# Kernel tuning notes

Measured on AMD Instinct MI355X. Metric: run time of the kernel, lower is better.

Reference implementation:

```python
import jax, jax.numpy as jnp
import numpy as np

B, Q, K, F, H, D = 2, 4096, 4096, 512, 8, 64

def setup_inputs() -> dict:
    key = jax.random.key(0)
    ks = jax.random.split(key, 6)
    s = 1.0 / np.sqrt(F)
    return {
        "inputs_q": jax.random.normal(ks[0], (B, Q, F), dtype=jnp.float32),
        "inputs_kv": jax.random.normal(ks[1], (B, K, F), dtype=jnp.float32),
        "Wq": jax.random.normal(ks[2], (F, H, D), dtype=jnp.float32) * s,
        "Wk": jax.random.normal(ks[3], (F, H, D), dtype=jnp.float32) * s,
        "Wv": jax.random.normal(ks[4], (F, H, D), dtype=jnp.float32) * s,
        "Wo": jax.random.normal(ks[5], (H, D, F), dtype=jnp.float32) * (1.0 / np.sqrt(H * D)),
    }

def reference(inputs_q, inputs_kv, Wq, Wk, Wv, Wo):
    # QKV projections (DenseGeneral, no bias): [B, L, F] -> [B, L, H, D]
    q = jnp.einsum("bqf,fhd->bqhd", inputs_q, Wq)
    k = jnp.einsum("bkf,fhd->bkhd", inputs_kv, Wk)
    v = jnp.einsum("bkf,fhd->bkhd", inputs_kv, Wv)
    # Explicit attention matrix [B, H, Q, K] as in the original module
    logits = jnp.einsum("bqhd,bkhd->bhqk", q, k)
    attn = jax.nn.softmax(logits, axis=-1)
    out = jnp.einsum("bhqk,bkhd->bqhd", attn, v)
    # Output projection over (heads, head_dim): [B, Q, H, D] -> [B, Q, F]
    return jnp.einsum("bqhd,hdf->bqf", out, Wo)
```

## Files before the change

### kernel.cpp

```cpp
#include <hip/hip_runtime.h>
#include <hip/hip_bf16.h>

typedef short bf16x8 __attribute__((ext_vector_type(8)));
typedef _Float16 f16;
typedef f16 f16x8 __attribute__((ext_vector_type(8)));
typedef float f32x4 __attribute__((ext_vector_type(4)));
typedef unsigned short u16;
typedef u16 u16x8 __attribute__((ext_vector_type(8)));
typedef unsigned int u32;
typedef u32 u32x2 __attribute__((ext_vector_type(2)));

#define B_  2
#define L_  4096
#define F_  512
#define H_  8
#define D_  64
#define M_  8192
#define NSPL 2
#define KHALF (L_ / NSPL)

#define LOG2E 1.442695041f

__device__ inline u16 f2bf(float f) {
    union { float f; unsigned u; } v; v.f = f;
    unsigned r = v.u + 0x7fff + ((v.u >> 16) & 1);
    return (u16)(r >> 16);
}
__device__ inline u16 f2h(float f) {
    union { f16 h; u16 u; } v; v.h = (f16)f;
    return v.u;
}
__device__ inline float h2f(u16 u) {
    union { u16 u; f16 h; } v; v.u = u;
    return (float)v.h;
}

__global__ __launch_bounds__(256) void wt_kernel(
    const float* __restrict__ Wq, const float* __restrict__ Wk,
    const float* __restrict__ Wv, const float* __restrict__ Wo,
    u16* __restrict__ Tq, u16* __restrict__ Tk,
    u16* __restrict__ Tv, u16* __restrict__ To) {
    __shared__ float t[32][33];
    const int z = blockIdx.z;
    const float* in = (z == 0) ? Wq : (z == 1) ? Wk : (z == 2) ? Wv : Wo;
    u16* out = (z == 0) ? Tq : (z == 1) ? Tk : (z == 2) ? Tv : To;
    int k0 = blockIdx.y * 32, n0 = blockIdx.x * 32;
    int c = threadIdx.x & 31, r8 = threadIdx.x >> 5;
#pragma unroll
    for (int i = 0; i < 4; ++i) {
        int r = r8 * 4 + i;
        t[r][c] = in[(size_t)(k0 + r) * F_ + n0 + c];
    }
    __syncthreads();
#pragma unroll
    for (int i = 0; i < 4; ++i) {
        int r = r8 * 4 + i;
        out[(size_t)(n0 + r) * F_ + k0 + c] = f2h(t[c][r]);
    }
}

__global__ __launch_bounds__(256, 3) void proj_kernel(
    const float* __restrict__ Xq, const float* __restrict__ Xkv,
    const u16* __restrict__ Wqt, const u16* __restrict__ Wkt,
    const u16* __restrict__ Wvt,
    u16* __restrict__ Qw, u16* __restrict__ Kw, u16* __restrict__ Vw) {
    __shared__ u16 Ah[128][72];
    __shared__ u16 B1[64][72];
    const int tid = threadIdx.x;
    const int w = tid >> 6, lane = tid & 63, lx = lane & 15, quad = lane >> 4;
    const int m0 = blockIdx.x * 128, n0 = blockIdx.y * 64;
    const int z = blockIdx.z;
    const float* A = (z == 0) ? Xq : Xkv;
    const u16* W1 = (z == 0) ? Wqt : (z == 1) ? Wkt : Wvt;

    float4 apre[8];
    u16x8 b1p[2];

    auto load_ab = [&](int k0) {
#pragma unroll
        for (int it = 0; it < 4; ++it) {
            int slot = tid + it * 256, r = slot >> 3, g = (slot & 7) * 8;
            apre[2 * it]     = *(const float4*)(A + (size_t)(m0 + r) * F_ + k0 + g);
            apre[2 * it + 1] = *(const float4*)(A + (size_t)(m0 + r) * F_ + k0 + g + 4);
        }
#pragma unroll
        for (int it = 0; it < 2; ++it) {
            int slot = tid + it * 256, r = slot >> 3, g = (slot & 7) * 8;
            b1p[it] = *(const u16x8*)(W1 + (size_t)(n0 + r) * F_ + k0 + g);
        }
    };
    auto write_ab = [&]() {
#pragma unroll
        for (int it = 0; it < 4; ++it) {
            int slot = tid + it * 256, r = slot >> 3, g = (slot & 7) * 8;
            float4 f0 = apre[2 * it], f1 = apre[2 * it + 1];
            u16 th[8] = {f2h(f0.x), f2h(f0.y), f2h(f0.z), f2h(f0.w),
                         f2h(f1.x), f2h(f1.y), f2h(f1.z), f2h(f1.w)};
            *(u16x8*)&Ah[r][g] = *(u16x8*)th;
        }
#pragma unroll
        for (int it = 0; it < 2; ++it) {
            int slot = tid + it * 256, r = slot >> 3, g = (slot & 7) * 8;
            *(u16x8*)&B1[r][g] = b1p[it];
        }
    };

    f32x4 acc1[2][4] = {};

    load_ab(0);
    write_ab();
    __syncthreads();
    load_ab(64);

    for (int k0 = 0; k0 < F_; k0 += 64) {
#pragma unroll
        for (int ks = 0; ks < 2; ++ks) {
            f16x8 af[2];
#pragma unroll
            for (int mf = 0; mf < 2; ++mf)
                af[mf] = *(const f16x8*)&Ah[w * 32 + mf * 16 + lx][ks * 32 + quad * 8];
#pragma unroll
            for (int nt = 0; nt < 4; ++nt) {
                f16x8 b1 = *(const f16x8*)&B1[nt * 16 + lx][ks * 32 + quad * 8];
#pragma unroll
                for (int mf = 0; mf < 2; ++mf)
                    acc1[mf][nt] = __builtin_amdgcn_mfma_f32_16x16x32_f16(af[mf], b1, acc1[mf][nt], 0, 0, 0);
            }
        }
        if (k0 < F_ - 64) {
            __syncthreads();
            write_ab();
            __syncthreads();
            if (k0 < F_ - 128) load_ab(k0 + 128);
        }
    }

    const int h = n0 >> 6;
    if (z < 2) {
        const float scl = (z == 0) ? LOG2E : 1.0f;
        u16* C1 = (z == 0) ? Qw : Kw;
#pragma unroll
        for (int mf = 0; mf < 2; ++mf)
#pragma unroll
            for (int nt = 0; nt < 4; ++nt)
#pragma unroll
                for (int i = 0; i < 4; ++i) {
                    int m = m0 + w * 32 + mf * 16 + quad * 4 + i;
                    int b = m >> 12, l = m & 4095;
                    int d = nt * 16 + lx;
                    C1[((size_t)(b * H_ + h) * L_ + l) * D_ + d] = f2h(acc1[mf][nt][i] * scl);
                }
    } else {
        __syncthreads();
#pragma unroll
        for (int mf = 0; mf < 2; ++mf)
#pragma unroll
            for (int nt = 0; nt < 4; ++nt)
#pragma unroll
                for (int i = 0; i < 4; ++i)
                    Ah[w * 32 + mf * 16 + quad * 4 + i][nt * 16 + lx] = f2bf(acc1[mf][nt][i]);
        __syncthreads();
        int d = tid >> 2, seg = (tid & 3) * 32;
        int b = m0 >> 12;
        u16 tmp[32];
#pragma unroll
        for (int j = 0; j < 32; ++j) tmp[j] = Ah[seg + j][d];
        size_t base = ((size_t)(b * H_ + h) * D_ + d) * L_ + (m0 & 4095) + seg;
#pragma unroll
        for (int c = 0; c < 4; ++c)
            *(u16x8*)(Vw + base + c * 8) = *(u16x8*)&tmp[c * 8];
    }
}

__global__ __launch_bounds__(256) void out_gemm(const u16* __restrict__ A16,
                                                const u16* __restrict__ Wt,
                                                float* __restrict__ Cf) {
    __shared__ u16 As[128][72];
    __shared__ u16 Bs[128][72];
    const int tid = threadIdx.x;
    const int w = tid >> 6, lane = tid & 63, lx = lane & 15, quad = lane >> 4;
    const int m0 = blockIdx.x * 128, n0 = blockIdx.y * 128;

    u16x8 a16p[4];
    u16x8 bp[4];

    auto load_ab = [&](int k0) {
#pragma unroll
        for (int it = 0; it < 4; ++it) {
            int slot = tid + it * 256, r = slot >> 3, g = (slot & 7) * 8;
            a16p[it] = *(const u16x8*)(A16 + (size_t)(m0 + r) * F_ + k0 + g);
            bp[it]   = *(const u16x8*)(Wt  + (size_t)(n0 + r) * F_ + k0 + g);
        }
    };
    auto write_ab = [&]() {
#pragma unroll
        for (int it = 0; it < 4; ++it) {
            int slot = tid + it * 256, r = slot >> 3, g = (slot & 7) * 8;
            *(u16x8*)&As[r][g] = a16p[it];
            *(u16x8*)&Bs[r][g] = bp[it];
        }
    };

    f32x4 acc[2][8] = {};

    load_ab(0);
    write_ab();
    __syncthreads();
    load_ab(64);

    for (int k0 = 0; k0 < F_; k0 += 64) {
#pragma unroll
        for (int ks = 0; ks < 2; ++ks) {
            f16x8 af[2];
#pragma unroll
            for (int mf = 0; mf < 2; ++mf)
                af[mf] = *(const f16x8*)&As[w * 32 + mf * 16 + lx][ks * 32 + quad * 8];
#pragma unroll
            for (int nt = 0; nt < 8; ++nt) {
                f16x8 bf = *(const f16x8*)&Bs[nt * 16 + lx][ks * 32 + quad * 8];
#pragma unroll
                for (int mf = 0; mf < 2; ++mf)
                    acc[mf][nt] = __builtin_amdgcn_mfma_f32_16x16x32_f16(af[mf], bf, acc[mf][nt], 0, 0, 0);
            }
        }
        if (k0 < F_ - 64) {
            __syncthreads();
            write_ab();
            __syncthreads();
            if (k0 < F_ - 128) load_ab(k0 + 128);
        }
    }

#pragma unroll
    for (int mf = 0; mf < 2; ++mf)
#pragma unroll
        for (int nt = 0; nt < 8; ++nt)
#pragma unroll
            for (int i = 0; i < 4; ++i) {
                int m = m0 + w * 32 + mf * 16 + quad * 4 + i;
                int n = n0 + nt * 16 + lx;
                Cf[(size_t)m * F_ + n] = acc[mf][nt][i];
            }
}

__global__ __launch_bounds__(256, 2) void flash_mfma(
    const u16* __restrict__ Qg, const u16* __restrict__ Kg,
    const u16* __restrict__ Vtg, u16* __restrict__ On, float* __restrict__ Ls) {
    __shared__ u16 Ks[2][64][72];
    __shared__ u16 Vs[2][64][72];

    const int tid = threadIdx.x;
    const int w = tid >> 6, lane = tid & 63, lx = lane & 15, quad = lane >> 4;

    const int x = blockIdx.x;
    const int t = x >> 3;
    const int hh = t >> 5;
    const int s = (t >> 4) & 1;
    const int bh = (x & 7) * 2 + hh;
    const int q0 = (t & 15) * 256;

    const u16* Qp = Qg + ((size_t)bh * L_ + q0) * D_;
    const u16* Kp = Kg + (size_t)bh * L_ * D_ + (size_t)(s * KHALF) * D_;
    const u16* Vp = Vtg + (size_t)bh * D_ * L_ + s * KHALF;

    f16x8 qreg[4][2];
#pragma unroll
    for (int qf = 0; qf < 4; ++qf)
#pragma unroll
        for (int ks = 0; ks < 2; ++ks)
            qreg[qf][ks] = *(const f16x8*)(Qp + (size_t)(w * 64 + qf * 16 + lx) * D_ +
                                           ks * 32 + quad * 8);

    u16x8 kp[2], vp[2];
    auto load_kv = [&](int kt) {
#pragma unroll
        for (int it = 0; it < 2; ++it) {
            int slot = tid + it * 256, r = slot >> 3, g = (slot & 7) * 8;
            kp[it] = *(const u16x8*)(Kp + (size_t)(kt * 64 + r) * D_ + g);
            vp[it] = *(const u16x8*)(Vp + (size_t)r * L_ + kt * 64 + g);
        }
    };
    auto write_kv = [&](int p) {
#pragma unroll
        for (int it = 0; it < 2; ++it) {
            int slot = tid + it * 256, r = slot >> 3, g = (slot & 7) * 8;
            *(u16x8*)&Ks[p][r][g] = kp[it];
            *(u16x8*)&Vs[p][r][g] = vp[it];
        }
    };

    auto smqf = [&](const f32x4& s0, const f32x4& s1) -> bf16x8 {
        u32 ub0[4], ub1[4];
#pragma unroll
        for (int i = 0; i < 4; ++i) {
            ub0[i] = __float_as_uint(__builtin_amdgcn_exp2f(s0[i]));
            ub1[i] = __float_as_uint(__builtin_amdgcn_exp2f(s1[i]));
        }
        u32 pu0 = __builtin_amdgcn_perm(ub0[1], ub0[0], 0x07060302u);
        u32 pw0 = __builtin_amdgcn_perm(ub0[3], ub0[2], 0x07060302u);
        u32 pu1 = __builtin_amdgcn_perm(ub1[1], ub1[0], 0x07060302u);
        u32 pw1 = __builtin_amdgcn_perm(ub1[3], ub1[2], 0x07060302u);
        u32x2 r  = __builtin_amdgcn_permlane32_swap(pu0, pu1, false, false);
        u32x2 r2 = __builtin_amdgcn_permlane16_swap(r[0], r[1], false, false);
        u32x2 tt = __builtin_amdgcn_permlane32_swap(pw0, pw1, false, false);
        u32x2 t2 = __builtin_amdgcn_permlane16_swap(tt[0], tt[1], false, false);
        union { u32 d[4]; bf16x8 h; } cvt;
        cvt.d[0] = r2[0];
        cvt.d[1] = t2[0];
        cvt.d[2] = r2[1];
        cvt.d[3] = t2[1];
        return cvt.h;
    };

    const bf16x8 vone = {0x3F80, 0x3F80, 0x3F80, 0x3F80,
                         0x3F80, 0x3F80, 0x3F80, 0x3F80};
    f32x4 o[4][4] = {};
    f32x4 osum[4] = {};

    load_kv(0);
    write_kv(0);
    __syncthreads();
    load_kv(1);

    const int NT = KHALF / 64;
    for (int kt = 0; kt < NT; ++kt) {
        const int p = kt & 1;

        f32x4 sv[4][4] = {};
#pragma unroll
        for (int ks = 0; ks < 2; ++ks)
#pragma unroll
            for (int nt = 0; nt < 2; ++nt) {
                f16x8 ak = *(const f16x8*)&Ks[p][nt * 16 + lx][ks * 32 + quad * 8];
#pragma unroll
                for (int qf = 0; qf < 4; ++qf)
                    sv[nt][qf] = __builtin_amdgcn_mfma_f32_16x16x32_f16(ak, qreg[qf][ks], sv[nt][qf], 0, 0, 0);
            }

        f16x8 akB[2][2];
#pragma unroll
        for (int ks = 0; ks < 2; ++ks)
#pragma unroll
            for (int nt = 0; nt < 2; ++nt)
                akB[ks][nt] = *(const f16x8*)&Ks[p][(nt + 2) * 16 + lx][ks * 32 + quad * 8];

        bf16x8 apA[4];
#pragma unroll
        for (int qf = 0; qf < 4; ++qf) {
            sv[2][qf] = __builtin_amdgcn_mfma_f32_16x16x32_f16(akB[0][0], qreg[qf][0], sv[2][qf], 0, 0, 0);
            sv[3][qf] = __builtin_amdgcn_mfma_f32_16x16x32_f16(akB[0][1], qreg[qf][0], sv[3][qf], 0, 0, 0);
            sv[2][qf] = __builtin_amdgcn_mfma_f32_16x16x32_f16(akB[1][0], qreg[qf][1], sv[2][qf], 0, 0, 0);
            sv[3][qf] = __builtin_amdgcn_mfma_f32_16x16x32_f16(akB[1][1], qreg[qf][1], sv[3][qf], 0, 0, 0);
            apA[qf] = smqf(sv[0][qf], sv[1][qf]);
        }

        if (kt < NT - 1) write_kv(p ^ 1);

        bf16x8 bvA[4];
#pragma unroll
        for (int nt = 0; nt < 4; ++nt)
            bvA[nt] = *(const bf16x8*)&Vs[p][nt * 16 + lx][quad * 8];

        __builtin_amdgcn_s_setprio(1);
        bf16x8 apB[4];
#pragma unroll
        for (int qf = 0; qf < 4; ++qf) {
            osum[qf] = __builtin_amdgcn_mfma_f32_16x16x32_bf16(apA[qf], vone, osum[qf], 0, 0, 0);
#pragma unroll
            for (int nt = 0; nt < 4; ++nt)
                o[qf][nt] = __builtin_amdgcn_mfma_f32_16x16x32_bf16(apA[qf], bvA[nt], o[qf][nt], 0, 0, 0);
            apB[qf] = smqf(sv[2][qf], sv[3][qf]);
        }

        bf16x8 bvB[4];
#pragma unroll
        for (int nt = 0; nt < 4; ++nt)
            bvB[nt] = *(const bf16x8*)&Vs[p][nt * 16 + lx][32 + quad * 8];
#pragma unroll
        for (int qf = 0; qf < 4; ++qf)
            osum[qf] = __builtin_amdgcn_mfma_f32_16x16x32_bf16(apB[qf], vone, osum[qf], 0, 0, 0);
#pragma unroll
        for (int nt = 0; nt < 4; ++nt) {
#pragma unroll
            for (int qf = 0; qf < 4; ++qf)
                o[qf][nt] = __builtin_amdgcn_mfma_f32_16x16x32_bf16(apB[qf], bvB[nt], o[qf][nt], 0, 0, 0);
        }
        __builtin_amdgcn_s_setprio(0);

        if (kt < NT - 1) __syncthreads();
        if (kt < NT - 2) load_kv(kt + 2);
    }

    const int b = bh >> 3, h = bh & 7;
    u16* Op = On + (size_t)s * M_ * F_;
#pragma unroll
    for (int qf = 0; qf < 4; ++qf) {
        float linv[4];
#pragma unroll
        for (int i = 0; i < 4; ++i) linv[i] = 1.f / osum[qf][i];
#pragma unroll
        for (int nt = 0; nt < 4; ++nt)
#pragma unroll
            for (int i = 0; i < 4; ++i) {
                int l = q0 + w * 64 + qf * 16 + quad * 4 + i;
                Op[((size_t)b * L_ + l) * (H_ * D_) + h * D_ + nt * 16 + lx] =
                    f2h(o[qf][nt][i] * linv[i]);
            }
        if (lx == 0) {
            float* lp = Ls + ((size_t)s * (B_ * H_) + bh) * L_ +
                        q0 + w * 64 + qf * 16 + quad * 4;
#pragma unroll
            for (int i = 0; i < 4; ++i) lp[i] = osum[qf][i];
        }
    }
}

__global__ __launch_bounds__(256) void reduce_kernel(
    const u16* __restrict__ On, const float* __restrict__ Ls,
    u16* __restrict__ Ow) {
    int gid = blockIdx.x * 256 + threadIdx.x;
    size_t off = (size_t)gid * 8;
    int row = gid >> 3;
    int b = row >> 15, rem = row & 32767;
    int l = rem >> 3, h = rem & 7;
    int lidx = ((b * H_ + h) << 12) + l;
    float l1 = Ls[lidx], l2 = Ls[B_ * H_ * L_ + lidx];
    float w1 = l1 / (l1 + l2), w2 = 1.f - w1;
    u16x8 a = *(const u16x8*)(On + off);
    u16x8 c = *(const u16x8*)(On + (size_t)M_ * F_ + off);
    u16 r[8];
#pragma unroll
    for (int j = 0; j < 8; ++j)
        r[j] = f2h(w1 * h2f(a[j]) + w2 * h2f(c[j]));
    *(u16x8*)(Ow + off) = *(u16x8*)r;
}

extern "C" void kernel_launch(void* const* d_in, const int* in_sizes, int n_in,
                              void* d_out, int out_size, void* d_ws, size_t ws_size,
                              hipStream_t stream)
{
    const float* Xq  = (const float*)d_in[0];
    const float* Xkv = (const float*)d_in[1];
    const float* Wq  = (const float*)d_in[2];
    const float* Wk  = (const float*)d_in[3];
    const float* Wv  = (const float*)d_in[4];
    const float* Wo  = (const float*)d_in[5];
    float* out = (float*)d_out;

    u16* ws  = (u16*)d_ws;
    const size_t MF = (size_t)M_ * F_;
    const size_t FF = (size_t)F_ * F_;
    u16* Wqt = ws;
    u16* Wkt = Wqt + FF;
    u16* Wvt = Wkt + FF;
    u16* Wot = Wvt + FF;
    u16* Qw  = Wot + FF;
    u16* Kw  = Qw + MF;
    u16* Vw  = Kw + MF;
    u16* On  = Vw + MF;
    float* Ls = (float*)(On + 2 * MF);
    u16* Ow  = Qw;

    wt_kernel<<<dim3(16, 16, 4), 256, 0, stream>>>(Wq, Wk, Wv, Wo,
                                                   Wqt, Wkt, Wvt, Wot);

    proj_kernel<<<dim3(64, 8, 3), 256, 0, stream>>>(Xq, Xkv, Wqt, Wkt, Wvt,
                                                    Qw, Kw, Vw);

    flash_mfma<<<dim3(512), 256, 0, stream>>>(Qw, Kw, Vw, On, Ls);

    reduce_kernel<<<dim3((int)(MF / 8 / 256)), 256, 0, stream>>>(On, Ls, Ow);

    out_gemm<<<dim3(64, 4), 256, 0, stream>>>(Ow, Wot, out);
}
```

Before: 198.4 us.

## Fuse K and V projections into one block sharing the input tile

The projection kernel now computes K and V in the same block, reusing the converted inputs_kv tile in shared memory against two weight tiles. This cuts the grid from three z-slices to two and halves the read and fp16 conversion of the KV input. In exchange the KV blocks carry more accumulators and shared memory, which may lower occupancy, and the two z-slices now do unequal work. Separately, the s_setprio raises around the PV MFMA section of the flash kernel are removed.

```diff
diff --git a/kernel.cpp b/kernel.cpp
--- a/kernel.cpp
+++ b/kernel.cpp
@@ -66,15 +66,16 @@
     u16* __restrict__ Qw, u16* __restrict__ Kw, u16* __restrict__ Vw) {
     __shared__ u16 Ah[128][72];
     __shared__ u16 B1[64][72];
+    __shared__ u16 B2[64][72];
     const int tid = threadIdx.x;
     const int w = tid >> 6, lane = tid & 63, lx = lane & 15, quad = lane >> 4;
     const int m0 = blockIdx.x * 128, n0 = blockIdx.y * 64;
-    const int z = blockIdx.z;
-    const float* A = (z == 0) ? Xq : Xkv;
-    const u16* W1 = (z == 0) ? Wqt : (z == 1) ? Wkt : Wvt;
+    const bool isKV = (blockIdx.z == 1);
+    const float* A = isKV ? Xkv : Xq;
+    const u16* W1 = isKV ? Wkt : Wqt;
 
     float4 apre[8];
-    u16x8 b1p[2];
+    u16x8 b1p[2], b2p[2];
 
     auto load_ab = [&](int k0) {
 #pragma unroll
@@ -87,6 +88,8 @@
         for (int it = 0; it < 2; ++it) {
             int slot = tid + it * 256, r = slot >> 3, g = (slot & 7) * 8;
             b1p[it] = *(const u16x8*)(W1 + (size_t)(n0 + r) * F_ + k0 + g);
+            if (isKV)
+                b2p[it] = *(const u16x8*)(Wvt + (size_t)(n0 + r) * F_ + k0 + g);
         }
     };
     auto write_ab = [&]() {
@@ -102,10 +105,11 @@
         for (int it = 0; it < 2; ++it) {
             int slot = tid + it * 256, r = slot >> 3, g = (slot & 7) * 8;
             *(u16x8*)&B1[r][g] = b1p[it];
-        }
-    };
-
-    f32x4 acc1[2][4] = {};
+            if (isKV) *(u16x8*)&B2[r][g] = b2p[it];
+        }
+    };
+
+    f32x4 acc1[2][4] = {}, acc2[2][4] = {};
 
     load_ab(0);
     write_ab();
@@ -125,6 +129,12 @@
 #pragma unroll
                 for (int mf = 0; mf < 2; ++mf)
                     acc1[mf][nt] = __builtin_amdgcn_mfma_f32_16x16x32_f16(af[mf], b1, acc1[mf][nt], 0, 0, 0);
+                if (isKV) {
+                    f16x8 b2 = *(const f16x8*)&B2[nt * 16 + lx][ks * 32 + quad * 8];
+#pragma unroll
+                    for (int mf = 0; mf < 2; ++mf)
+                        acc2[mf][nt] = __builtin_amdgcn_mfma_f32_16x16x32_f16(af[mf], b2, acc2[mf][nt], 0, 0, 0);
+                }
             }
         }
         if (k0 < F_ - 64) {
@@ -136,29 +146,28 @@
     }
 
     const int h = n0 >> 6;
-    if (z < 2) {
-        const float scl = (z == 0) ? LOG2E : 1.0f;
-        u16* C1 = (z == 0) ? Qw : Kw;
+    const float scl = isKV ? 1.0f : LOG2E;
+    u16* C1 = isKV ? Kw : Qw;
+#pragma unroll
+    for (int mf = 0; mf < 2; ++mf)
+#pragma unroll
+        for (int nt = 0; nt < 4; ++nt)
+#pragma unroll
+            for (int i = 0; i < 4; ++i) {
+                int m = m0 + w * 32 + mf * 16 + quad * 4 + i;
+                int b = m >> 12, l = m & 4095;
+                int d = nt * 16 + lx;
+                C1[((size_t)(b * H_ + h) * L_ + l) * D_ + d] = f2h(acc1[mf][nt][i] * scl);
+            }
+    if (isKV) {
+        __syncthreads();
 #pragma unroll
         for (int mf = 0; mf < 2; ++mf)
 #pragma unroll
             for (int nt = 0; nt < 4; ++nt)
 #pragma unroll
-                for (int i = 0; i < 4; ++i) {
-                    int m = m0 + w * 32 + mf * 16 + quad * 4 + i;
-                    int b = m >> 12, l = m & 4095;
-                    int d = nt * 16 + lx;
-                    C1[((size_t)(b * H_ + h) * L_ + l) * D_ + d] = f2h(acc1[mf][nt][i] * scl);
-                }
-    } else {
-        __syncthreads();
-#pragma unroll
-        for (int mf = 0; mf < 2; ++mf)
-#pragma unroll
-            for (int nt = 0; nt < 4; ++nt)
-#pragma unroll
                 for (int i = 0; i < 4; ++i)
-                    Ah[w * 32 + mf * 16 + quad * 4 + i][nt * 16 + lx] = f2bf(acc1[mf][nt][i]);
+                    Ah[w * 32 + mf * 16 + quad * 4 + i][nt * 16 + lx] = f2bf(acc2[mf][nt][i]);
         __syncthreads();
         int d = tid >> 2, seg = (tid & 3) * 32;
         int b = m0 >> 12;
@@ -361,7 +370,6 @@
         for (int nt = 0; nt < 4; ++nt)
             bvA[nt] = *(const bf16x8*)&Vs[p][nt * 16 + lx][quad * 8];
 
-        __builtin_amdgcn_s_setprio(1);
         bf16x8 apB[4];
 #pragma unroll
         for (int qf = 0; qf < 4; ++qf) {
@@ -385,7 +393,6 @@
             for (int qf = 0; qf < 4; ++qf)
                 o[qf][nt] = __builtin_amdgcn_mfma_f32_16x16x32_bf16(apB[qf], bvB[nt], o[qf][nt], 0, 0, 0);
         }
-        __builtin_amdgcn_s_setprio(0);
 
         if (kt < NT - 1) __syncthreads();
         if (kt < NT - 2) load_kv(kt + 2);
@@ -464,7 +471,7 @@
     wt_kernel<<<dim3(16, 16, 4), 256, 0, stream>>>(Wq, Wk, Wv, Wo,
                                                    Wqt, Wkt, Wvt, Wot);
 
-    proj_kernel<<<dim3(64, 8, 3), 256, 0, stream>>>(Xq, Xkv, Wqt, Wkt, Wvt,
+    proj_kernel<<<dim3(64, 8, 2), 256, 0, stream>>>(Xq, Xkv, Wqt, Wkt, Wvt,
                                                     Qw, Kw, Vw);
 
     flash_mfma<<<dim3(512), 256, 0, stream>>>(Qw, Kw, Vw, On, Ls);
```

After: 201.9 us. Within noise of the previous version (+1.8%).
